# Kernel optimization log

Measured on AMD Instinct MI355X. Metric: run time of the kernel, lower is better.

## Reference

```python
import jax, jax.numpy as jnp
import numpy as np
from jax import lax

STRIDE = (1, 1)
PADDING = ((1, 1), (1, 1))  # padding=1 for 3x3 kernel -> same spatial size


def _conv_one(xi, wi, bi):
    # xi: [C_in, H, W], wi: [C_out, C_in, k, k], bi: [C_out]
    out = lax.conv_general_dilated(
        xi[None], wi, window_strides=STRIDE, padding=PADDING,
        dimension_numbers=('NCHW', 'OIHW', 'NCHW'))
    return out[0] + bi[:, None, None]


def setup_inputs() -> dict:
    key = jax.random.key(0)
    k1, k2, k3, k4 = jax.random.split(key, 4)
    B, C_in, H, W = 16, 64, 128, 128
    C_out, K, ks = 64, 5, 3
    x = jax.random.normal(k1, (B, C_in, H, W), dtype=jnp.float32)
    weights = jax.random.uniform(k2, (B, K), dtype=jnp.float32)  # attention over K kernels
    Wbank = jax.random.normal(k3, (K, C_out, C_in, ks, ks), dtype=jnp.float32)
    bbank = jax.random.normal(k4, (K, C_out), dtype=jnp.float32) * 0.1
    return {"x": x, "weights": weights, "Wbank": Wbank, "bbank": bbank}


def reference(x, weights, Wbank, bbank):
    # Per-sample aggregated kernels: [B, C_out, C_in, k, k]
    agg_w = jnp.einsum('bk,koihw->boihw', weights, Wbank)
    # Per-sample aggregated bias: [B, C_out]
    agg_b = weights @ bbank
    # Grouped conv with groups = batch, expressed as vmapped per-sample conv
    return jax.vmap(_conv_one)(x, agg_w, agg_b)
```

## Files before the change

kernel.cpp:

```cpp
#include <hip/hip_runtime.h>
#include <hip/hip_bf16.h>


typedef __attribute__((ext_vector_type(8))) __bf16 bf16x8;
typedef __attribute__((ext_vector_type(16))) float f32x16;
typedef __attribute__((ext_vector_type(4))) unsigned int u32x4;

#define NB 16
#define CI 64
#define CO 64
#define HH 128
#define WW 128
#define KBANK 5
#define ASTR 36864

__device__ __forceinline__ unsigned short f2bfu(float f) {
    __hip_bfloat16 h = __float2bfloat16(f);
    unsigned short s;
    __builtin_memcpy(&s, &h, 2);
    return s;
}

__global__ void prep_kernel(const float* __restrict__ weights,
                            const float* __restrict__ Wbank,
                            const float* __restrict__ bbank,
                            short* __restrict__ aggw,
                            float* __restrict__ aggb) {
    int idx = blockIdx.x * 256 + threadIdx.x;
    int b   = idx / ASTR;
    int rem = idx - b * ASTR;
    int j   = rem & 7;
    int co5 = (rem >> 3) & 31;
    int g   = (rem >> 8) & 1;
    int mk  = rem >> 9;
    int m   = mk / 36;
    int ks  = mk - m * 36;
    int co  = m * 32 + co5;
    int k   = ks * 16 + g * 8 + j;
    int tap = k >> 6;
    int ci  = k & 63;
    float s = 0.f;
#pragma unroll
    for (int kk = 0; kk < KBANK; ++kk)
        s += weights[b * KBANK + kk] * Wbank[((kk * CO + co) * CI + ci) * 9 + tap];
    aggw[idx] = (short)f2bfu(s);
    if (k == 0) {
        float sb = 0.f;
#pragma unroll
        for (int kk = 0; kk < KBANK; ++kk)
            sb += weights[b * KBANK + kk] * bbank[kk * CO + co];
        aggb[b * CO + co] = sb;
    }
}

#define WAITV(N) asm volatile("s_waitcnt vmcnt(" #N ")" ::: "memory")
#define WAITL0   asm volatile("s_waitcnt lgkmcnt(0)" ::: "memory")
#define SBAR     do { __builtin_amdgcn_s_barrier(); __builtin_amdgcn_sched_barrier(0); } while (0)

__global__ __launch_bounds__(512, 2) void conv_kernel(const float* __restrict__ x,
                                                      const short* __restrict__ aggw,
                                                      const float* __restrict__ aggb,
                                                      float* __restrict__ out) {
    __shared__ short bring[4][8][130][8];
    __shared__ float fring[2][64][128];

    const int t   = threadIdx.x;
    const int lin = blockIdx.x;
    const int b   = (lin & 7) * 2 + ((lin >> 3) & 1);
    const int r0  = (lin >> 4) * 8;

    const int l  = t & 63;
    const int wv = t >> 6;
    const int m  = wv >> 2;
    const int nq = wv & 3;
    const int lm = l & 31;
    const int g  = l >> 5;

    const float* xb = x + (size_t)b * CI * HH * WW;
    const short* Ab = aggw + (size_t)b * ASTR + (size_t)m * 36 * 512;

    bf16x8 A[36];
#pragma unroll
    for (int ks = 0; ks < 36; ++ks)
        A[ks] = *(const bf16x8*)(Ab + ks * 512 + l * 8);

    float bias[16];
#pragma unroll
    for (int rg = 0; rg < 16; ++rg)
        bias[rg] = aggb[b * CO + m * 32 + (rg & 3) + 8 * (rg >> 2) + 4 * g];

    if (t < 64) {
        int slot = t >> 4, ch = (t >> 1) & 7, px = (t & 1) * 129;
        *(u32x4*)&bring[slot][ch][px][0] = u32x4{0u, 0u, 0u, 0u};
    }

    auto stage = [&](int r, int fs) {
        float* fbase = &fring[fs][0][0];
#pragma unroll
        for (int i = 0; i < 4; ++i) {
            int c  = i * 512 + t;
            int ci = c >> 5;
            int w  = (c & 31) * 4;
            const float* src = xb + ((size_t)ci * HH + r) * WW + w;
            float* dst = fbase + (size_t)(i * 512 + (t & ~63)) * 4;
            __builtin_amdgcn_global_load_lds(
                (const __attribute__((address_space(1))) void*)src,
                (__attribute__((address_space(3))) void*)dst, 16, 0, 0);
        }
    };

    auto convertz = [&](const float* fbase, int bs, bool zero) {
#pragma unroll
        for (int k2 = 0; k2 < 2; ++k2) {
            int c   = k2 * 512 + t;
            int ch  = c >> 7;
            int pix = (c & 127) + 1;
            unsigned u0 = 0, u1 = 0, u2 = 0, u3 = 0;
            if (!zero) {
                const float* p = fbase + ch * 1024 + (pix - 1);
                u0 = (unsigned)f2bfu(p[0])   | ((unsigned)f2bfu(p[128]) << 16);
                u1 = (unsigned)f2bfu(p[256]) | ((unsigned)f2bfu(p[384]) << 16);
                u2 = (unsigned)f2bfu(p[512]) | ((unsigned)f2bfu(p[640]) << 16);
                u3 = (unsigned)f2bfu(p[768]) | ((unsigned)f2bfu(p[896]) << 16);
            }
            *(u32x4*)&bring[bs][ch][pix][0] = u32x4{u0, u1, u2, u3};
        }
    };

    if (r0 > 0) stage(r0 - 1, 0);
    stage(r0, 1);
    WAITV(4); SBAR;
    if (r0 > 0) convertz(&fring[0][0][0], 0, false);
    else        convertz(nullptr,         0, true);
    WAITL0; SBAR;
    stage(r0 + 1, 0);
    WAITV(4); SBAR;
    convertz(&fring[1][0][0], 1, false);
    WAITL0; SBAR;
    stage(r0 + 2, 1);
    WAITV(4); SBAR;
    convertz(&fring[0][0][0], 2, false);
    WAITV(0);
    WAITL0; SBAR;

#pragma unroll
    for (int s = 0; s < 8; ++s) {
        const int r = r0 + s;

        if (r + 2 <= 127) convertz(&fring[(s + 1) & 1][0][0], (s + 3) & 3, false);
        else              convertz(nullptr,                   (s + 3) & 3, true);

        if (r + 3 <= 127) stage(r + 3, s & 1);

        f32x16 acc = (f32x16)0.0f;
#pragma unroll
        for (int ks = 0; ks < 36; ++ks) {
            const int tap = ks >> 2, q = ks & 3;
            const int dy = tap / 3, dx = tap - dy * 3;
            const short* sb = &bring[(s + dy) & 3][0][0][0];
            const int pix = nq * 32 + dx + lm;
            bf16x8 bv = *(const bf16x8*)&sb[((q * 2 + g) * 130 + pix) * 8];
            acc = __builtin_amdgcn_mfma_f32_32x32x16_bf16(A[ks], bv, acc, 0, 0, 0);
        }

        const int wc = nq * 32 + lm;
#pragma unroll
        for (int rg = 0; rg < 16; ++rg) {
            int co = m * 32 + (rg & 3) + 8 * (rg >> 2) + 4 * g;
            out[(((size_t)b * CO + co) * HH + r) * WW + wc] = acc[rg] + bias[rg];
        }

        WAITV(16);
        WAITL0;
        SBAR;
    }
}

extern "C" void kernel_launch(void* const* d_in, const int* in_sizes, int n_in,
                              void* d_out, int out_size, void* d_ws, size_t ws_size,
                              hipStream_t stream) {
    const float* x       = (const float*)d_in[0];
    const float* weights = (const float*)d_in[1];
    const float* Wbank   = (const float*)d_in[2];
    const float* bbank   = (const float*)d_in[3];
    float* out = (float*)d_out;

    short* aggw = (short*)d_ws;
    float* aggb = (float*)((char*)d_ws + 1179648);

    prep_kernel<<<dim3((NB * ASTR) / 256), dim3(256), 0, stream>>>(weights, Wbank, bbank, aggw, aggb);
    conv_kernel<<<dim3(256), dim3(512), 0, stream>>>(x, aggw, aggb, out);
}
```

Before: 40.24 us.

## Compute two output rows per step sharing B-fragment loads across a 5-slot ring

Result: slower. 61.53 us (+52.9%).

```diff
diff --git a/kernel.cpp b/kernel.cpp
--- a/kernel.cpp
+++ b/kernel.cpp
@@ -53,15 +53,17 @@
     }
 }
 
-#define WAITV(N) asm volatile("s_waitcnt vmcnt(" #N ")" ::: "memory")
-#define WAITL0   asm volatile("s_waitcnt lgkmcnt(0)" ::: "memory")
-#define SBAR     do { __builtin_amdgcn_s_barrier(); __builtin_amdgcn_sched_barrier(0); } while (0)
+#define WAITVN(N) asm volatile("s_waitcnt vmcnt(" #N ")" ::: "memory")
+#define WAITL0    asm volatile("s_waitcnt lgkmcnt(0)" ::: "memory")
+#define SBAR      do { __builtin_amdgcn_s_barrier(); __builtin_amdgcn_sched_barrier(0); } while (0)
+
+template <int N> struct ic { static constexpr int v = N; };
 
 __global__ __launch_bounds__(512, 2) void conv_kernel(const float* __restrict__ x,
                                                       const short* __restrict__ aggw,
                                                       const float* __restrict__ aggb,
                                                       float* __restrict__ out) {
-    __shared__ short bring[4][8][130][8];
+    __shared__ short bring[5][8][130][8];
     __shared__ float fring[2][64][128];
 
     const int t   = threadIdx.x;
@@ -89,7 +91,7 @@
     for (int rg = 0; rg < 16; ++rg)
         bias[rg] = aggb[b * CO + m * 32 + (rg & 3) + 8 * (rg >> 2) + 4 * g];
 
-    if (t < 64) {
+    if (t < 80) {
         int slot = t >> 4, ch = (t >> 1) & 7, px = (t & 1) * 129;
         *(u32x4*)&bring[slot][ch][px][0] = u32x4{0u, 0u, 0u, 0u};
     }
@@ -108,8 +110,8 @@
                 (__attribute__((address_space(3))) void*)dst, 16, 0, 0);
         }
     };
-
-    auto convertz = [&](const float* fbase, int bs, bool zero) {
+    auto convz = [&](int fs, int bs, bool zero) {
+        const float* fbase = &fring[fs][0][0];
 #pragma unroll
         for (int k2 = 0; k2 < 2; ++k2) {
             int c   = k2 * 512 + t;
@@ -127,53 +129,102 @@
         }
     };
 
-    if (r0 > 0) stage(r0 - 1, 0);
+    stage(r0 > 0 ? r0 - 1 : 0, 0);
     stage(r0, 1);
-    WAITV(4); SBAR;
-    if (r0 > 0) convertz(&fring[0][0][0], 0, false);
-    else        convertz(nullptr,         0, true);
+    WAITVN(4); SBAR;
+    convz(0, 0, r0 == 0);
+    WAITVN(0); WAITL0; SBAR;
+    convz(1, 1, false);
+    stage(r0 + 1, 0);
     WAITL0; SBAR;
-    stage(r0 + 1, 0);
-    WAITV(4); SBAR;
-    convertz(&fring[1][0][0], 1, false);
+    WAITVN(0); SBAR;
+    convz(0, 2, false);
+    stage(r0 + 2, 1);
     WAITL0; SBAR;
-    stage(r0 + 2, 1);
-    WAITV(4); SBAR;
-    convertz(&fring[0][0][0], 2, false);
-    WAITV(0);
-    WAITL0; SBAR;
-
-#pragma unroll
-    for (int s = 0; s < 8; ++s) {
-        const int r = r0 + s;
-
-        if (r + 2 <= 127) convertz(&fring[(s + 1) & 1][0][0], (s + 3) & 3, false);
-        else              convertz(nullptr,                   (s + 3) & 3, true);
-
-        if (r + 3 <= 127) stage(r + 3, s & 1);
-
-        f32x16 acc = (f32x16)0.0f;
-#pragma unroll
-        for (int ks = 0; ks < 36; ++ks) {
-            const int tap = ks >> 2, q = ks & 3;
-            const int dy = tap / 3, dx = tap - dy * 3;
-            const short* sb = &bring[(s + dy) & 3][0][0][0];
-            const int pix = nq * 32 + dx + lm;
-            bf16x8 bv = *(const bf16x8*)&sb[((q * 2 + g) * 130 + pix) * 8];
-            acc = __builtin_amdgcn_mfma_f32_32x32x16_bf16(A[ks], bv, acc, 0, 0, 0);
-        }
-
-        const int wc = nq * 32 + lm;
+    WAITVN(0); SBAR;
+    convz(1, 3, false);
+    WAITL0;
+    stage(r0 + 3, 0);
+    SBAR;
+    stage(r0 + 4, 1);
+
+    auto stepf = [&](auto Sc) {
+        constexpr int s = decltype(Sc)::v;
+        const int r = r0 + 2 * s;
+        const int pixb = nq * 32 + lm;
+
+        if constexpr (s < 3) {
+            if constexpr (s == 0) { WAITVN(4); } else { WAITVN(36); }
+            convz(0, (2 * s + 4) % 5, false);
+        }
+
+        f32x16 acc0 = (f32x16)0.0f;
+        f32x16 acc1 = (f32x16)0.0f;
+
+        {
+            const short* sb = &bring[(2 * s) % 5][0][0][0];
+#pragma unroll
+            for (int dx = 0; dx < 3; ++dx)
+#pragma unroll
+                for (int q = 0; q < 4; ++q) {
+                    bf16x8 bv = *(const bf16x8*)&sb[((q * 2 + g) * 130 + pixb + dx) * 8];
+                    acc0 = __builtin_amdgcn_mfma_f32_32x32x16_bf16(A[dx * 4 + q], bv, acc0, 0, 0, 0);
+                }
+        }
+
+        if constexpr (s < 3) {
+            WAITL0; SBAR;
+            if constexpr (s == 0) { WAITVN(0); } else { WAITVN(32); }
+            convz(1, (2 * s) % 5, (r0 + 2 * s + 4) > 127);
+            if constexpr (s < 2) stage(r + 5, 0);
+        }
+
+#pragma unroll
+        for (int o = 1; o <= 2; ++o) {
+            const short* sb = &bring[(2 * s + o) % 5][0][0][0];
+#pragma unroll
+            for (int dx = 0; dx < 3; ++dx)
+#pragma unroll
+                for (int q = 0; q < 4; ++q) {
+                    bf16x8 bv = *(const bf16x8*)&sb[((q * 2 + g) * 130 + pixb + dx) * 8];
+                    acc0 = __builtin_amdgcn_mfma_f32_32x32x16_bf16(A[(o * 3 + dx) * 4 + q], bv, acc0, 0, 0, 0);
+                    acc1 = __builtin_amdgcn_mfma_f32_32x32x16_bf16(A[((o - 1) * 3 + dx) * 4 + q], bv, acc1, 0, 0, 0);
+                }
+        }
+        {
+            const short* sb = &bring[(2 * s + 3) % 5][0][0][0];
+#pragma unroll
+            for (int dx = 0; dx < 3; ++dx)
+#pragma unroll
+                for (int q = 0; q < 4; ++q) {
+                    bf16x8 bv = *(const bf16x8*)&sb[((q * 2 + g) * 130 + pixb + dx) * 8];
+                    acc1 = __builtin_amdgcn_mfma_f32_32x32x16_bf16(A[(6 + dx) * 4 + q], bv, acc1, 0, 0, 0);
+                }
+        }
+
+        if constexpr (s < 3) { WAITL0; SBAR; }
+        if constexpr (s < 2) {
+            int r6 = r + 6; if (r6 > 127) r6 = 127;
+            stage(r6, 1);
+        }
+
+        const int wc = pixb;
 #pragma unroll
         for (int rg = 0; rg < 16; ++rg) {
             int co = m * 32 + (rg & 3) + 8 * (rg >> 2) + 4 * g;
-            out[(((size_t)b * CO + co) * HH + r) * WW + wc] = acc[rg] + bias[rg];
-        }
-
-        WAITV(16);
-        WAITL0;
-        SBAR;
-    }
+            out[(((size_t)b * CO + co) * HH + r) * WW + wc] = acc0[rg] + bias[rg];
+        }
+#pragma unroll
+        for (int rg = 0; rg < 16; ++rg) {
+            int co = m * 32 + (rg & 3) + 8 * (rg >> 2) + 4 * g;
+            out[(((size_t)b * CO + co) * HH + (r + 1)) * WW + wc] = acc1[rg] + bias[rg];
+        }
+    };
+
+    stepf(ic<0>{});
+    stepf(ic<1>{});
+    stepf(ic<2>{});
+    stepf(ic<3>{});
 }
 
 extern "C" void kernel_launch(void* const* d_in, const int* in_sizes, int n_in,
```
